# Performance work log

Measured on AMD Instinct MI355X. Metric: run time of the kernel, lower is better.

Reference implementation:

```python
import jax, jax.numpy as jnp
import numpy as np

B, S, D, H = 4, 4096, 128, 128

def setup_inputs() -> dict:
    key = jax.random.key(0)
    ks = jax.random.split(key, 7)
    sd = 1.0 / np.sqrt(D)
    return {
        "x": jax.random.normal(ks[0], (B, S, D), dtype=jnp.float32),
        "Wq": jax.random.normal(ks[1], (D, H), dtype=jnp.float32) * sd,
        "bq": jax.random.normal(ks[2], (H,), dtype=jnp.float32) * sd,
        "Wk": jax.random.normal(ks[3], (D, H), dtype=jnp.float32) * sd,
        "bk": jax.random.normal(ks[4], (H,), dtype=jnp.float32) * sd,
        "Wv": jax.random.normal(ks[5], (D, D), dtype=jnp.float32) * sd,
        "bv": jax.random.normal(ks[6], (D,), dtype=jnp.float32) * sd,
    }

def reference(x, Wq, bq, Wk, bk, Wv, bv):
    # Q,K: [B,S,H]; V: [B,S,D]
    Q = jnp.einsum('bsd,dh->bsh', x, Wq) + bq
    K = jnp.einsum('bsd,dh->bsh', x, Wk) + bk
    V = jnp.einsum('bsd,de->bse', x, Wv) + bv
    scale = jnp.sqrt(jnp.asarray(H, dtype=x.dtype))
    scores = jnp.einsum('bqh,bkh->bqk', Q, K) / scale  # [B,S,S]
    attn = jax.nn.softmax(scores, axis=-1)             # dropout = identity (eval mode)
    context = jnp.einsum('bqk,bkd->bqd', attn, V)      # [B,S,D]
    return context.mean(axis=1)                        # [B,D]
```

## Files before the change

### kernel.cpp

```cpp
#include <hip/hip_runtime.h>

#define SLEN 4096
#define DDIM 128
#define BATCH 4
#define QB 256
#define NQB (SLEN / QB)
#define NW 4
#define KSPLIT 8
#define NTILES (SLEN / 16)
#define TPB (NTILES / KSPLIT)
#define STAGE_TILES 4
#define NSTAGES (TPB / STAGE_TILES)
#define WSLABS (NQB * NW)
#define SCLOG2E 0.12751743f

typedef __bf16 v8bf __attribute__((ext_vector_type(8)));
typedef float f32x4 __attribute__((ext_vector_type(4)));

__device__ __forceinline__ f32x4 mfma16(v8bf a, v8bf b, f32x4 c) {
  return __builtin_amdgcn_mfma_f32_16x16x32_bf16(a, b, c, 0, 0, 0);
}

__device__ __forceinline__ void gload_lds16(const void* g, void* l) {
  __builtin_amdgcn_global_load_lds(
      (const __attribute__((address_space(1))) unsigned int*)g,
      (__attribute__((address_space(3))) unsigned int*)l, 16, 0, 0);
}

__device__ __forceinline__ void stage_k(const __bf16* __restrict__ Krow0,
                                        char* buf, int wave, int lane) {
#pragma unroll
  for (int i = 0; i < 4; ++i) {
    int s = i * 256 + wave * 64 + lane;
    int r = s >> 4;
    int p = s & 15;
    int lsl = p ^ (r & 7);
    const __bf16* src = Krow0 + (size_t)r * DDIM + lsl * 8;
    char* dst = buf + (size_t)(i * 256 + wave * 64) * 16;
    gload_lds16(src, dst);
  }
}

__global__ __launch_bounds__(256) void k0_wt(const float* __restrict__ Wq,
                                             const float* __restrict__ Wk,
                                             __bf16* __restrict__ Wt) {
  int idx = blockIdx.x * 256 + threadIdx.x;
  int ct = idx >> 8;
  int hs = (idx >> 6) & 3;
  int l  = idx & 63;
  int col = ((ct & 7) << 4) + (l & 15);
  const float* W = (ct < 8) ? Wq : Wk;
  int hbase = hs * 32 + (l >> 4) * 8;
  __bf16* dst = Wt + (size_t)idx * 8;
  for (int i = 0; i < 8; ++i)
    dst[i] = (__bf16)W[(hbase + i) * DDIM + col];
}

__global__ __launch_bounds__(256) void k1_proj(const float* __restrict__ x,
                                               const __bf16* __restrict__ Wt,
                                               const float* __restrict__ bq,
                                               const float* __restrict__ bk,
                                               __bf16* __restrict__ Qb,
                                               __bf16* __restrict__ Kb) {
  int wave = threadIdx.x >> 6, lane = threadIdx.x & 63;
  int lr = lane & 15, lg = lane >> 4;
  int r0 = blockIdx.x * 64 + wave * 16;
  const float* xrow = x + (size_t)(r0 + lr) * DDIM;

  v8bf xf[4];
#pragma unroll
  for (int hs = 0; hs < 4; ++hs) {
    float4 a = *reinterpret_cast<const float4*>(xrow + hs * 32 + lg * 8);
    float4 c = *reinterpret_cast<const float4*>(xrow + hs * 32 + lg * 8 + 4);
    v8bf t;
    t[0] = (__bf16)a.x; t[1] = (__bf16)a.y; t[2] = (__bf16)a.z; t[3] = (__bf16)a.w;
    t[4] = (__bf16)c.x; t[5] = (__bf16)c.y; t[6] = (__bf16)c.z; t[7] = (__bf16)c.w;
    xf[hs] = t;
  }

  for (int ct = 0; ct < 16; ++ct) {
    f32x4 acc = {0.f, 0.f, 0.f, 0.f};
#pragma unroll
    for (int hs = 0; hs < 4; ++hs) {
      v8bf wf = *reinterpret_cast<const v8bf*>(Wt + ((size_t)(ct * 4 + hs) * 64 + lane) * 8);
      acc = mfma16(xf[hs], wf, acc);
    }
    int col = ((ct & 7) << 4) + lr;
    float bias = (ct < 8) ? bq[col] : bk[col];
    __bf16* dst = (ct < 8) ? Qb : Kb;
#pragma unroll
    for (int j = 0; j < 4; ++j) {
      int row = r0 + lg * 4 + j;
      dst[(size_t)row * DDIM + col] = (__bf16)(acc[j] + bias);
    }
  }
}

__global__ __launch_bounds__(256, 2) void k2a_z(const __bf16* __restrict__ Qb,
                                                const __bf16* __restrict__ Kb,
                                                float* __restrict__ zpart) {
  int b = blockIdx.y, qblk = blockIdx.x, ks = blockIdx.z;
  int wave = threadIdx.x >> 6, lane = threadIdx.x & 63;
  int lr = lane & 15, lg = lane >> 4;

  __shared__ __align__(16) char kbuf[2][STAGE_TILES * 16 * 256];

  const __bf16* Qbase = Qb + ((size_t)b * SLEN + qblk * QB + wave * 64) * DDIM;
  const __bf16* Kbase = Kb + ((size_t)b * SLEN + ks * TPB * 16) * DDIM;

  stage_k(Kbase, kbuf[0], wave, lane);

  v8bf qf[4][4];
#pragma unroll
  for (int qs = 0; qs < 4; ++qs)
#pragma unroll
    for (int hs = 0; hs < 4; ++hs)
      qf[qs][hs] = *reinterpret_cast<const v8bf*>(Qbase + (size_t)(qs * 16 + lr) * DDIM + hs * 32 + lg * 8);

  float zacc[4][4];
#pragma unroll
  for (int qs = 0; qs < 4; ++qs)
#pragma unroll
    for (int j = 0; j < 4; ++j) zacc[qs][j] = 0.f;

  __syncthreads();

  for (int s = 0; s < NSTAGES; ++s) {
    if (s + 1 < NSTAGES)
      stage_k(Kbase + (size_t)(s + 1) * STAGE_TILES * 16 * DDIM, kbuf[(s + 1) & 1], wave, lane);
    const char* buf = kbuf[s & 1];
#pragma unroll
    for (int t = 0; t < STAGE_TILES; ++t) {
      int r = t * 16 + lr;
      int rowbase = r * 256;
      f32x4 acc[4];
#pragma unroll
      for (int qs = 0; qs < 4; ++qs) acc[qs] = (f32x4){0.f, 0.f, 0.f, 0.f};
#pragma unroll
      for (int hs = 0; hs < 4; ++hs) {
        int slot = (hs * 4 + lg) ^ (r & 7);
        v8bf kc = *reinterpret_cast<const v8bf*>(buf + rowbase + slot * 16);
#pragma unroll
        for (int qs = 0; qs < 4; ++qs) acc[qs] = mfma16(qf[qs][hs], kc, acc[qs]);
      }
#pragma unroll
      for (int qs = 0; qs < 4; ++qs)
#pragma unroll
        for (int j = 0; j < 4; ++j)
          zacc[qs][j] += exp2f(acc[qs][j] * SCLOG2E);
    }
    __syncthreads();
  }

#pragma unroll
  for (int qs = 0; qs < 4; ++qs)
#pragma unroll
    for (int j = 0; j < 4; ++j) {
      float z = zacc[qs][j];
      z += __shfl_xor(z, 1);
      z += __shfl_xor(z, 2);
      z += __shfl_xor(z, 4);
      z += __shfl_xor(z, 8);
      if (lr == 0)
        zpart[(((size_t)b * NQB + qblk) * KSPLIT + ks) * QB + wave * 64 + qs * 16 + lg * 4 + j] = z;
    }
}

__global__ __launch_bounds__(256, 2) void k2c_w(const __bf16* __restrict__ Qb,
                                                const __bf16* __restrict__ Kb,
                                                const float* __restrict__ zpart,
                                                __bf16* __restrict__ wpart) {
  int b = blockIdx.y, qblk = blockIdx.x, ks = blockIdx.z;
  int wave = threadIdx.x >> 6, lane = threadIdx.x & 63;
  int lr = lane & 15, lg = lane >> 4;

  __shared__ __align__(16) char kbuf[2][STAGE_TILES * 16 * 256];
  __shared__ float invZ[QB];

  const __bf16* Qbase = Qb + ((size_t)b * SLEN + qblk * QB + wave * 64) * DDIM;
  const __bf16* Kbase = Kb + ((size_t)b * SLEN + ks * TPB * 16) * DDIM;

  stage_k(Kbase, kbuf[0], wave, lane);

  v8bf qf[4][4];
#pragma unroll
  for (int qs = 0; qs < 4; ++qs)
#pragma unroll
    for (int hs = 0; hs < 4; ++hs)
      qf[qs][hs] = *reinterpret_cast<const v8bf*>(Qbase + (size_t)(qs * 16 + lr) * DDIM + hs * 32 + lg * 8);

  {
    const float* zp = zpart + ((size_t)b * NQB + qblk) * KSPLIT * QB + threadIdx.x;
    float z = 0.f;
#pragma unroll
    for (int s = 0; s < KSPLIT; ++s) z += zp[(size_t)s * QB];
    invZ[threadIdx.x] = 1.0f / z;
  }

  __syncthreads();

  float iz[4][4];
#pragma unroll
  for (int qs = 0; qs < 4; ++qs)
#pragma unroll
    for (int j = 0; j < 4; ++j)
      iz[qs][j] = invZ[wave * 64 + qs * 16 + lg * 4 + j];

  __bf16* wrow = wpart + ((size_t)b * WSLABS + qblk * NW + wave) * SLEN + ks * TPB * 16;

  for (int s = 0; s < NSTAGES; ++s) {
    if (s + 1 < NSTAGES)
      stage_k(Kbase + (size_t)(s + 1) * STAGE_TILES * 16 * DDIM, kbuf[(s + 1) & 1], wave, lane);
    const char* buf = kbuf[s & 1];
#pragma unroll
    for (int t = 0; t < STAGE_TILES; ++t) {
      int r = t * 16 + lr;
      int rowbase = r * 256;
      f32x4 acc[4];
#pragma unroll
      for (int qs = 0; qs < 4; ++qs) acc[qs] = (f32x4){0.f, 0.f, 0.f, 0.f};
#pragma unroll
      for (int hs = 0; hs < 4; ++hs) {
        int slot = (hs * 4 + lg) ^ (r & 7);
        v8bf kc = *reinterpret_cast<const v8bf*>(buf + rowbase + slot * 16);
#pragma unroll
        for (int qs = 0; qs < 4; ++qs) acc[qs] = mfma16(qf[qs][hs], kc, acc[qs]);
      }
      float wk = 0.f;
#pragma unroll
      for (int qs = 0; qs < 4; ++qs)
#pragma unroll
        for (int j = 0; j < 4; ++j)
          wk += exp2f(acc[qs][j] * SCLOG2E) * iz[qs][j];
      wk += __shfl_xor(wk, 16);
      wk += __shfl_xor(wk, 32);
      if (lg == 0)
        wrow[(s * STAGE_TILES + t) * 16 + lr] = (__bf16)wk;
    }
    __syncthreads();
  }
}

__global__ __launch_bounds__(128) void k4_u(const float* __restrict__ x,
                                            const __bf16* __restrict__ wpart,
                                            float* __restrict__ upart) {
  int b = blockIdx.y, c = blockIdx.x, d = threadIdx.x;
  __shared__ float ws[128];
  const __bf16* p = wpart + (size_t)b * WSLABS * SLEN + c * 128 + d;
  float s = 0.f;
  for (int j = 0; j < WSLABS; ++j) s += (float)p[(size_t)j * SLEN];
  ws[d] = s;
  __syncthreads();
  const float* xb = x + ((size_t)b * SLEN + c * 128) * DDIM;
  float acc = 0.f;
  for (int kk = 0; kk < 128; ++kk)
    acc += ws[kk] * xb[(size_t)kk * DDIM + d];
  upart[((size_t)b * 32 + c) * DDIM + d] = acc;
}

__global__ __launch_bounds__(128) void k5_out(const float* __restrict__ upart,
                                              const float* __restrict__ Wv,
                                              const float* __restrict__ bv,
                                              float* __restrict__ out) {
  int b = blockIdx.x, d = threadIdx.x;
  __shared__ float u[DDIM];
  float s = 0.f;
  for (int c = 0; c < 32; ++c) s += upart[((size_t)b * 32 + c) * DDIM + d];
  u[d] = s;
  __syncthreads();
  float acc = 0.f;
  for (int dp = 0; dp < DDIM; ++dp) acc += u[dp] * Wv[(size_t)dp * DDIM + d];
  out[b * DDIM + d] = acc * (1.0f / SLEN) + bv[d];
}

extern "C" void kernel_launch(void* const* d_in, const int* in_sizes, int n_in,
                              void* d_out, int out_size, void* d_ws, size_t ws_size,
                              hipStream_t stream) {
  const float* x  = (const float*)d_in[0];
  const float* Wq = (const float*)d_in[1];
  const float* bq = (const float*)d_in[2];
  const float* Wk = (const float*)d_in[3];
  const float* bk = (const float*)d_in[4];
  const float* Wv = (const float*)d_in[5];
  const float* bv = (const float*)d_in[6];
  float* out = (float*)d_out;

  char* ws = (char*)d_ws;
  __bf16* Qb    = (__bf16*)(ws);
  __bf16* Kb    = (__bf16*)(ws + (4u << 20));
  __bf16* Wt    = (__bf16*)(ws + (8u << 20));
  __bf16* wpart = (__bf16*)(ws + (8u << 20) + (128u << 10));
  float*  zpart = (float*)(ws + (11u << 20) + (128u << 10));
  float*  upart = (float*)(ws + (11u << 20) + (704u << 10));

  k0_wt  <<<16, 256, 0, stream>>>(Wq, Wk, Wt);
  k1_proj<<<256, 256, 0, stream>>>(x, Wt, bq, bk, Qb, Kb);
  k2a_z  <<<dim3(NQB, BATCH, KSPLIT), 256, 0, stream>>>(Qb, Kb, zpart);
  k2c_w  <<<dim3(NQB, BATCH, KSPLIT), 256, 0, stream>>>(Qb, Kb, zpart, wpart);
  k4_u   <<<dim3(32, BATCH), 128, 0, stream>>>(x, wpart, upart);
  k5_out <<<BATCH, 128, 0, stream>>>(upart, Wv, bv, out);
}
```

Baseline: 89.91 us.

## Stage full K slab in LDS once and sweep Q rows over it

The attention-score kernels now give each block a 256-row K slab staged into LDS once (64KB) and loop each wave over two 64-row Q tiles, replacing the double-buffered streaming of K across a 512-key split. The column-weight kernel reduces its per-key weights across waves in shared memory and writes one fp32 partial per (batch, 512-query group) instead of per-wave bf16 slabs, which shrinks the k4 reduction from 64 to 8 slabs. A flat grid with XCD-aware block decoding is added to group blocks sharing K/Q. The larger LDS footprint may limit occupancy, and dropping the double buffer loses load/compute overlap.

```diff
diff --git a/kernel.cpp b/kernel.cpp
--- a/kernel.cpp
+++ b/kernel.cpp
@@ -3,15 +3,12 @@
 #define SLEN 4096
 #define DDIM 128
 #define BATCH 4
-#define QB 256
-#define NQB (SLEN / QB)
+#define KROWS 256
+#define NKB (SLEN / KROWS)
+#define QROWS 512
+#define NQR (SLEN / QROWS)
 #define NW 4
-#define KSPLIT 8
-#define NTILES (SLEN / 16)
-#define TPB (NTILES / KSPLIT)
-#define STAGE_TILES 4
-#define NSTAGES (TPB / STAGE_TILES)
-#define WSLABS (NQB * NW)
+#define NPASS 2
 #define SCLOG2E 0.12751743f
 
 typedef __bf16 v8bf __attribute__((ext_vector_type(8)));
@@ -27,16 +24,25 @@
       (__attribute__((address_space(3))) unsigned int*)l, 16, 0, 0);
 }
 
-__device__ __forceinline__ void stage_k(const __bf16* __restrict__ Krow0,
-                                        char* buf, int wave, int lane) {
-#pragma unroll
-  for (int i = 0; i < 4; ++i) {
-    int s = i * 256 + wave * 64 + lane;
+__device__ __forceinline__ void decode_bid(int bid, int& b, int& qr, int& kblk) {
+  int x = bid & 7;
+  int i = bid >> 3;
+  int p = x * 4 + (i >> 4);
+  kblk = i & 15;
+  b = p >> 3;
+  qr = p & 7;
+}
+
+__device__ __forceinline__ void stage_kslab(const __bf16* __restrict__ Krow0,
+                                            char* buf, int wave, int lane) {
+#pragma unroll
+  for (int it = 0; it < 16; ++it) {
+    int s = it * 256 + wave * 64 + lane;
     int r = s >> 4;
-    int p = s & 15;
-    int lsl = p ^ (r & 7);
+    int pp = s & 15;
+    int lsl = pp ^ (r & 7);
     const __bf16* src = Krow0 + (size_t)r * DDIM + lsl * 8;
-    char* dst = buf + (size_t)(i * 256 + wave * 64) * 16;
+    char* dst = buf + (size_t)(it * 256 + wave * 64) * 16;
     gload_lds16(src, dst);
   }
 }
@@ -99,47 +105,44 @@
 __global__ __launch_bounds__(256, 2) void k2a_z(const __bf16* __restrict__ Qb,
                                                 const __bf16* __restrict__ Kb,
                                                 float* __restrict__ zpart) {
-  int b = blockIdx.y, qblk = blockIdx.x, ks = blockIdx.z;
+  int b, qr, kblk;
+  decode_bid(blockIdx.x, b, qr, kblk);
+  int p = b * NQR + qr;
   int wave = threadIdx.x >> 6, lane = threadIdx.x & 63;
   int lr = lane & 15, lg = lane >> 4;
 
-  __shared__ __align__(16) char kbuf[2][STAGE_TILES * 16 * 256];
-
-  const __bf16* Qbase = Qb + ((size_t)b * SLEN + qblk * QB + wave * 64) * DDIM;
-  const __bf16* Kbase = Kb + ((size_t)b * SLEN + ks * TPB * 16) * DDIM;
-
-  stage_k(Kbase, kbuf[0], wave, lane);
-
-  v8bf qf[4][4];
-#pragma unroll
-  for (int qs = 0; qs < 4; ++qs)
-#pragma unroll
-    for (int hs = 0; hs < 4; ++hs)
-      qf[qs][hs] = *reinterpret_cast<const v8bf*>(Qbase + (size_t)(qs * 16 + lr) * DDIM + hs * 32 + lg * 8);
-
-  float zacc[4][4];
-#pragma unroll
-  for (int qs = 0; qs < 4; ++qs)
-#pragma unroll
-    for (int j = 0; j < 4; ++j) zacc[qs][j] = 0.f;
-
-  __syncthreads();
-
-  for (int s = 0; s < NSTAGES; ++s) {
-    if (s + 1 < NSTAGES)
-      stage_k(Kbase + (size_t)(s + 1) * STAGE_TILES * 16 * DDIM, kbuf[(s + 1) & 1], wave, lane);
-    const char* buf = kbuf[s & 1];
-#pragma unroll
-    for (int t = 0; t < STAGE_TILES; ++t) {
-      int r = t * 16 + lr;
-      int rowbase = r * 256;
+  __shared__ __align__(16) char kbuf[KROWS * 256];
+
+  stage_kslab(Kb + ((size_t)b * SLEN + kblk * KROWS) * DDIM, kbuf, wave, lane);
+  __syncthreads();
+
+  for (int pass = 0; pass < NPASS; ++pass) {
+    int qloc0 = (wave * NPASS + pass) * 64;
+    const __bf16* Qp = Qb + ((size_t)b * SLEN + qr * QROWS + qloc0) * DDIM;
+
+    v8bf qf[4][4];
+#pragma unroll
+    for (int qs = 0; qs < 4; ++qs)
+#pragma unroll
+      for (int hs = 0; hs < 4; ++hs)
+        qf[qs][hs] = *reinterpret_cast<const v8bf*>(Qp + (size_t)(qs * 16 + lr) * DDIM + hs * 32 + lg * 8);
+
+    float zacc[4][4];
+#pragma unroll
+    for (int qs = 0; qs < 4; ++qs)
+#pragma unroll
+      for (int j = 0; j < 4; ++j) zacc[qs][j] = 0.f;
+
+#pragma unroll
+    for (int kt = 0; kt < KROWS / 16; ++kt) {
+      int rowbase = (kt * 16 + lr) * 256;
       f32x4 acc[4];
 #pragma unroll
       for (int qs = 0; qs < 4; ++qs) acc[qs] = (f32x4){0.f, 0.f, 0.f, 0.f};
 #pragma unroll
       for (int hs = 0; hs < 4; ++hs) {
-        int slot = (hs * 4 + lg) ^ (r & 7);
-        v8bf kc = *reinterpret_cast<const v8bf*>(buf + rowbase + slot * 16);
+        int slot = (hs * 4 + lg) ^ (lr & 7);
+        v8bf kc = *reinterpret_cast<const v8bf*>(kbuf + rowbase + slot * 16);
 #pragma unroll
         for (int qs = 0; qs < 4; ++qs) acc[qs] = mfma16(qf[qs][hs], kc, acc[qs]);
       }
@@ -149,80 +152,79 @@
         for (int j = 0; j < 4; ++j)
           zacc[qs][j] += exp2f(acc[qs][j] * SCLOG2E);
     }
-    __syncthreads();
-  }
-
-#pragma unroll
-  for (int qs = 0; qs < 4; ++qs)
-#pragma unroll
-    for (int j = 0; j < 4; ++j) {
-      float z = zacc[qs][j];
-      z += __shfl_xor(z, 1);
-      z += __shfl_xor(z, 2);
-      z += __shfl_xor(z, 4);
-      z += __shfl_xor(z, 8);
-      if (lr == 0)
-        zpart[(((size_t)b * NQB + qblk) * KSPLIT + ks) * QB + wave * 64 + qs * 16 + lg * 4 + j] = z;
-    }
+
+#pragma unroll
+    for (int qs = 0; qs < 4; ++qs)
+#pragma unroll
+      for (int j = 0; j < 4; ++j) {
+        float z = zacc[qs][j];
+        z += __shfl_xor(z, 1);
+        z += __shfl_xor(z, 2);
+        z += __shfl_xor(z, 4);
+        z += __shfl_xor(z, 8);
+        if (lr == 0)
+          zpart[((size_t)p * NKB + kblk) * QROWS + qloc0 + qs * 16 + lg * 4 + j] = z;
+      }
+  }
 }
 
 __global__ __launch_bounds__(256, 2) void k2c_w(const __bf16* __restrict__ Qb,
                                                 const __bf16* __restrict__ Kb,
                                                 const float* __restrict__ zpart,
-                                                __bf16* __restrict__ wpart) {
-  int b = blockIdx.y, qblk = blockIdx.x, ks = blockIdx.z;
+                                                float* __restrict__ wpart) {
+  int b, qr, kblk;
+  decode_bid(blockIdx.x, b, qr, kblk);
+  int p = b * NQR + qr;
   int wave = threadIdx.x >> 6, lane = threadIdx.x & 63;
   int lr = lane & 15, lg = lane >> 4;
 
-  __shared__ __align__(16) char kbuf[2][STAGE_TILES * 16 * 256];
-  __shared__ float invZ[QB];
-
-  const __bf16* Qbase = Qb + ((size_t)b * SLEN + qblk * QB + wave * 64) * DDIM;
-  const __bf16* Kbase = Kb + ((size_t)b * SLEN + ks * TPB * 16) * DDIM;
-
-  stage_k(Kbase, kbuf[0], wave, lane);
-
-  v8bf qf[4][4];
-#pragma unroll
-  for (int qs = 0; qs < 4; ++qs)
-#pragma unroll
-    for (int hs = 0; hs < 4; ++hs)
-      qf[qs][hs] = *reinterpret_cast<const v8bf*>(Qbase + (size_t)(qs * 16 + lr) * DDIM + hs * 32 + lg * 8);
-
-  {
-    const float* zp = zpart + ((size_t)b * NQB + qblk) * KSPLIT * QB + threadIdx.x;
+  __shared__ __align__(16) char kbuf[KROWS * 256];
+  __shared__ float invZ[QROWS];
+  __shared__ float warr[NW][KROWS];
+
+  stage_kslab(Kb + ((size_t)b * SLEN + kblk * KROWS) * DDIM, kbuf, wave, lane);
+
+  for (int q = threadIdx.x; q < QROWS; q += 256) {
+    const float* zp = zpart + (size_t)p * NKB * QROWS + q;
     float z = 0.f;
 #pragma unroll
-    for (int s = 0; s < KSPLIT; ++s) z += zp[(size_t)s * QB];
-    invZ[threadIdx.x] = 1.0f / z;
-  }
-
-  __syncthreads();
-
-  float iz[4][4];
-#pragma unroll
-  for (int qs = 0; qs < 4; ++qs)
-#pragma unroll
-    for (int j = 0; j < 4; ++j)
-      iz[qs][j] = invZ[wave * 64 + qs * 16 + lg * 4 + j];
-
-  __bf16* wrow = wpart + ((size_t)b * WSLABS + qblk * NW + wave) * SLEN + ks * TPB * 16;
-
-  for (int s = 0; s < NSTAGES; ++s) {
-    if (s + 1 < NSTAGES)
-      stage_k(Kbase + (size_t)(s + 1) * STAGE_TILES * 16 * DDIM, kbuf[(s + 1) & 1], wave, lane);
-    const char* buf = kbuf[s & 1];
-#pragma unroll
-    for (int t = 0; t < STAGE_TILES; ++t) {
-      int r = t * 16 + lr;
-      int rowbase = r * 256;
+    for (int kb = 0; kb < NKB; ++kb) z += zp[(size_t)kb * QROWS];
+    invZ[q] = 1.0f / z;
+  }
+  __syncthreads();
+
+  float wkacc[KROWS / 16];
+#pragma unroll
+  for (int kt = 0; kt < KROWS / 16; ++kt) wkacc[kt] = 0.f;
+
+  for (int pass = 0; pass < NPASS; ++pass) {
+    int qloc0 = (wave * NPASS + pass) * 64;
+    const __bf16* Qp = Qb + ((size_t)b * SLEN + qr * QROWS + qloc0) * DDIM;
+
+    v8bf qf[4][4];
+#pragma unroll
+    for (int qs = 0; qs < 4; ++qs)
+#pragma unroll
+      for (int hs = 0; hs < 4; ++hs)
+        qf[qs][hs] = *reinterpret_cast<const v8bf*>(Qp + (size_t)(qs * 16 + lr) * DDIM + hs * 32 + lg * 8);
+
+    float iz[4][4];
+#pragma unroll
+    for (int qs = 0; qs < 4; ++qs)
+#pragma unroll
+      for (int j = 0; j < 4; ++j)
+        iz[qs][j] = invZ[qloc0 + qs * 16 + lg * 4 + j];
+
+#pragma unroll
+    for (int kt = 0; kt < KROWS / 16; ++kt) {
+      int rowbase = (kt * 16 + lr) * 256;
       f32x4 acc[4];
 #pragma unroll
       for (int qs = 0; qs < 4; ++qs) acc[qs] = (f32x4){0.f, 0.f, 0.f, 0.f};
 #pragma unroll
       for (int hs = 0; hs < 4; ++hs) {
-        int slot = (hs * 4 + lg) ^ (r & 7);
-        v8bf kc = *reinterpret_cast<const v8bf*>(buf + rowbase + slot * 16);
+        int slot = (hs * 4 + lg) ^ (lr & 7);
+        v8bf kc = *reinterpret_cast<const v8bf*>(kbuf + rowbase + slot * 16);
 #pragma unroll
         for (int qs = 0; qs < 4; ++qs) acc[qs] = mfma16(qf[qs][hs], kc, acc[qs]);
       }
@@ -232,23 +234,33 @@
 #pragma unroll
         for (int j = 0; j < 4; ++j)
           wk += exp2f(acc[qs][j] * SCLOG2E) * iz[qs][j];
-      wk += __shfl_xor(wk, 16);
-      wk += __shfl_xor(wk, 32);
-      if (lg == 0)
-        wrow[(s * STAGE_TILES + t) * 16 + lr] = (__bf16)wk;
+      wkacc[kt] += wk;
     }
-    __syncthreads();
+  }
+
+#pragma unroll
+  for (int kt = 0; kt < KROWS / 16; ++kt) {
+    float wv = wkacc[kt];
+    wv += __shfl_xor(wv, 16);
+    wv += __shfl_xor(wv, 32);
+    if (lg == 0) warr[wave][kt * 16 + lr] = wv;
+  }
+  __syncthreads();
+  for (int k = threadIdx.x; k < KROWS; k += 256) {
+    float s = warr[0][k] + warr[1][k] + warr[2][k] + warr[3][k];
+    wpart[(size_t)p * SLEN + kblk * KROWS + k] = s;
   }
 }
 
 __global__ __launch_bounds__(128) void k4_u(const float* __restrict__ x,
-                                            const __bf16* __restrict__ wpart,
+                                            const float* __restrict__ wpart,
                                             float* __restrict__ upart) {
   int b = blockIdx.y, c = blockIdx.x, d = threadIdx.x;
   __shared__ float ws[128];
-  const __bf16* p = wpart + (size_t)b * WSLABS * SLEN + c * 128 + d;
+  const float* pw = wpart + (size_t)b * NQR * SLEN + c * 128 + d;
   float s = 0.f;
-  for (int j = 0; j < WSLABS; ++j) s += (float)p[(size_t)j * SLEN];
+#pragma unroll
+  for (int j = 0; j < NQR; ++j) s += pw[(size_t)j * SLEN];
   ws[d] = s;
   __syncthreads();
   const float* xb = x + ((size_t)b * SLEN + c * 128) * DDIM;
@@ -289,14 +301,14 @@
   __bf16* Qb    = (__bf16*)(ws);
   __bf16* Kb    = (__bf16*)(ws + (4u << 20));
   __bf16* Wt    = (__bf16*)(ws + (8u << 20));
-  __bf16* wpart = (__bf16*)(ws + (8u << 20) + (128u << 10));
-  float*  zpart = (float*)(ws + (11u << 20) + (128u << 10));
-  float*  upart = (float*)(ws + (11u << 20) + (704u << 10));
+  float*  zpart = (float*)(ws + (8u << 20) + (64u << 10));
+  float*  wpart = (float*)(ws + (9u << 20) + (64u << 10));
+  float*  upart = (float*)(ws + (10u << 20));
 
   k0_wt  <<<16, 256, 0, stream>>>(Wq, Wk, Wt);
   k1_proj<<<256, 256, 0, stream>>>(x, Wt, bq, bk, Qb, Kb);
-  k2a_z  <<<dim3(NQB, BATCH, KSPLIT), 256, 0, stream>>>(Qb, Kb, zpart);
-  k2c_w  <<<dim3(NQB, BATCH, KSPLIT), 256, 0, stream>>>(Qb, Kb, zpart, wpart);
+  k2a_z  <<<NKB * NQR * BATCH, 256, 0, stream>>>(Qb, Kb, zpart);
+  k2c_w  <<<NKB * NQR * BATCH, 256, 0, stream>>>(Qb, Kb, zpart, wpart);
   k4_u   <<<dim3(32, BATCH), 128, 0, stream>>>(x, wpart, upart);
   k5_out <<<BATCH, 128, 0, stream>>>(upart, Wv, bv, out);
 }
```

New measurement: 301.8 us. 236% more time.
